# Kernel tuning notes

Measured on AMD Instinct MI355X. Metric: run time of the kernel, lower is better.

## Reference

```python
import jax, jax.numpy as jnp
import numpy as np

TEMPERATURE = 0.1
NEG_INF = -1e30

def _normalize(v):
    # torch.nn.functional.normalize: v / max(||v||, 1e-12)
    n = jnp.linalg.norm(v, axis=-1, keepdims=True)
    return v / jnp.maximum(n, 1e-12)

def _line_loss(xn, yn, mx, my):
    # xn, yn: [T, D] normalized; mx, my: [T] {0,1} combined selection masks
    T = xn.shape[0]
    sim = (xn @ yn.T) / TEMPERATURE                     # [T, T]
    nx = jnp.sum(mx)
    ny = jnp.sum(my)
    # stable argsort puts selected indices first, preserving original order
    r = jnp.argsort(1 - mx)
    c = jnp.argsort(1 - my)
    sim_sel = sim[r][:, c]                              # selected block is top-left [nx, ny]
    ids = jnp.arange(T)
    masked = jnp.where((ids < nx)[:, None], sim_sel, NEG_INF)
    lse = jax.nn.logsumexp(masked, axis=0)              # column logsumexp over selected rows
    per = lse - jnp.diagonal(sim_sel)                   # = -log(exp(diag)/sum_col exp)
    m = jnp.minimum(nx, ny)                             # torch.diag length of [nx, ny] matrix
    return jnp.sum(jnp.where(ids < m, per, 0.0)) / m

def setup_inputs() -> dict:
    key = jax.random.key(0)
    k1, k2, k3, k4 = jax.random.split(key, 4)
    B, T, D = 8, 4096, 64
    x = jax.random.normal(k1, (B, T, D), dtype=jnp.float32)
    y = jax.random.normal(k2, (B, T, D), dtype=jnp.float32)
    image_masks1 = jax.random.randint(k3, (B, T), 0, 2).astype(jnp.int32)
    image_masks2 = jax.random.randint(k4, (B, T), 0, 2).astype(jnp.int32)
    shift_masks1 = jnp.ones((B, T), dtype=jnp.int32)
    shift_masks2 = jnp.ones((B, T), dtype=jnp.int32)
    return {"x": x, "y": y, "image_masks1": image_masks1, "image_masks2": image_masks2,
            "shift_masks1": shift_masks1, "shift_masks2": shift_masks2}

def reference(x, y, image_masks1, image_masks2, shift_masks1, shift_masks2):
    xn = _normalize(x)
    yn = _normalize(y)
    mx = shift_masks1 * image_masks1   # combined row selection (shift then image)
    my = shift_masks2 * image_masks2   # combined col selection
    losses = jax.vmap(_line_loss)(xn, yn, mx, my)  # [B]
    return jnp.mean(losses)
```

## Files before the change

### kernel.cpp

```cpp
#include <hip/hip_runtime.h>
#include <hip/hip_bf16.h>
#include <math.h>

#define T_DIM 4096
#define D_DIM 64
#define SPLITS 4
#define ROWS_PER_SPLIT (T_DIM / SPLITS)
#define ITERS (ROWS_PER_SPLIT / 64)

typedef short bfrag8 __attribute__((ext_vector_type(8)));
typedef float floatx4 __attribute__((ext_vector_type(4)));

__device__ __forceinline__ float bf2f(unsigned short u) {
    return __uint_as_float(((unsigned int)u) << 16);
}

__global__ void normalize_rows(const float* __restrict__ x, const float* __restrict__ y,
                               __hip_bfloat16* __restrict__ xn, __hip_bfloat16* __restrict__ yn,
                               int rows_per_tensor) {
    int gtid = blockIdx.x * blockDim.x + threadIdx.x;
    int row  = gtid >> 6;
    int lane = gtid & 63;
    const float* src; __hip_bfloat16* dst; float scale;
    if (row < rows_per_tensor) { src = x; dst = xn; scale = 10.0f; }
    else { src = y; dst = yn; scale = 1.0f; row -= rows_per_tensor; }
    size_t off = (size_t)row * D_DIM + lane;
    float v = src[off];
    float ss = v * v;
    #pragma unroll
    for (int o = 1; o < 64; o <<= 1) ss += __shfl_xor(ss, o);
    float inv = scale / fmaxf(sqrtf(ss), 1e-12f);
    dst[off] = __float2bfloat16(v * inv);
}

__global__ void compact_mask(const int* __restrict__ im1, const int* __restrict__ sh1,
                             const int* __restrict__ im2, const int* __restrict__ sh2,
                             int* __restrict__ Ridx, int* __restrict__ Cidx,
                             float* __restrict__ mxf, int* __restrict__ cnt, int B) {
    int z = blockIdx.x;
    int which = z & 1, b = z >> 1;
    const int* im = which ? im2 : im1;
    const int* sh = which ? sh2 : sh1;
    int* idxout   = which ? Cidx : Ridx;

    __shared__ int wtot[16];
    __shared__ int woff[16];
    __shared__ int sbase;
    int tid = threadIdx.x, w = tid >> 6, lane = tid & 63;
    if (tid == 0) sbase = 0;

    for (int chunk = 0; chunk < T_DIM; chunk += 1024) {
        int t = chunk + tid;
        int mv = im[(size_t)b * T_DIM + t] * sh[(size_t)b * T_DIM + t];
        unsigned long long bal = __ballot(mv != 0);
        int pre = __popcll(bal & ((1ull << lane) - 1ull));
        if (lane == 0) wtot[w] = __popcll(bal);
        __syncthreads();
        if (tid == 0) {
            int s = sbase;
            #pragma unroll
            for (int i = 0; i < 16; i++) { woff[i] = s; s += wtot[i]; }
            sbase = s;
        }
        __syncthreads();
        if (mv) idxout[(size_t)b * T_DIM + woff[w] + pre] = t;
        if (which == 0) mxf[(size_t)b * T_DIM + t] = (mv != 0) ? 1.0f : 0.0f;
    }
    __syncthreads();
    if (tid == 0) cnt[which * B + b] = sbase;
}

__launch_bounds__(256)
__global__ void ntxent_main(const __hip_bfloat16* __restrict__ xn,
                            const __hip_bfloat16* __restrict__ yn,
                            const float* __restrict__ mxf,
                            const int* __restrict__ Cidx,
                            const int* __restrict__ cnt,
                            float* __restrict__ gsum, int B) {
    int b  = blockIdx.y;
    int nx = cnt[b];
    int ny = cnt[B + b];
    int m  = min(nx, ny);
    int j0 = blockIdx.x * 64;
    if (j0 >= m) return;
    int rbase = blockIdx.z * ROWS_PER_SPLIT;

    __shared__ __hip_bfloat16 Bs[64 * 72];
    __shared__ float sum_exp[64];
    __shared__ int   Cloc[64];

    int tid  = threadIdx.x;
    int wave = tid >> 6, lane = tid & 63, quad = lane >> 4, c16 = lane & 15;

    if (tid < 64) {
        int j = j0 + tid;
        Cloc[tid]    = (j < ny) ? Cidx[(size_t)b * T_DIM + j] : 0;
        sum_exp[tid] = 0.0f;
    }
    __syncthreads();

    #pragma unroll
    for (int i = tid; i < 64 * 8; i += 256) {
        int c = i >> 3, part = i & 7;
        bfrag8 v = *reinterpret_cast<const bfrag8*>(
            yn + ((size_t)b * T_DIM + Cloc[c]) * D_DIM + part * 8);
        *reinterpret_cast<bfrag8*>(&Bs[c * 72 + part * 8]) = v;
    }
    __syncthreads();

    bfrag8 bf[4][2];
    #pragma unroll
    for (int cg = 0; cg < 4; cg++)
        #pragma unroll
        for (int kh = 0; kh < 2; kh++)
            bf[cg][kh] = *reinterpret_cast<const bfrag8*>(
                &Bs[(cg * 16 + c16) * 72 + kh * 32 + quad * 8]);

    const __hip_bfloat16* xb = xn + (size_t)b * T_DIM * D_DIM;
    const float* mb = mxf + (size_t)b * T_DIM;

    float csum[4] = {0.f, 0.f, 0.f, 0.f};

    const __hip_bfloat16* arow = xb + (size_t)(rbase + wave * 16 + c16) * D_DIM;
    bfrag8 af0 = *reinterpret_cast<const bfrag8*>(arow + quad * 8);
    bfrag8 af1 = *reinterpret_cast<const bfrag8*>(arow + 32 + quad * 8);
    float4 mv  = *reinterpret_cast<const float4*>(mb + rbase + wave * 16 + quad * 4);

    for (int it = 0; it < ITERS; it++) {
        int it1 = (it + 1) & (ITERS - 1);
        const __hip_bfloat16* narow =
            xb + (size_t)(rbase + it1 * 64 + wave * 16 + c16) * D_DIM;
        bfrag8 naf0 = *reinterpret_cast<const bfrag8*>(narow + quad * 8);
        bfrag8 naf1 = *reinterpret_cast<const bfrag8*>(narow + 32 + quad * 8);
        float4 nmv  = *reinterpret_cast<const float4*>(
            mb + rbase + it1 * 64 + wave * 16 + quad * 4);

        float mvv[4] = {mv.x, mv.y, mv.z, mv.w};
        #pragma unroll
        for (int cg = 0; cg < 4; cg++) {
            floatx4 acc = {0.f, 0.f, 0.f, 0.f};
            acc = __builtin_amdgcn_mfma_f32_16x16x32_bf16(af0, bf[cg][0], acc, 0, 0, 0);
            acc = __builtin_amdgcn_mfma_f32_16x16x32_bf16(af1, bf[cg][1], acc, 0, 0, 0);
            #pragma unroll
            for (int r = 0; r < 4; r++)
                csum[cg] += mvv[r] * __expf(acc[r]);
        }
        af0 = naf0; af1 = naf1; mv = nmv;
    }

    #pragma unroll
    for (int cg = 0; cg < 4; cg++) {
        csum[cg] += __shfl_xor(csum[cg], 16);
        csum[cg] += __shfl_xor(csum[cg], 32);
    }
    if (lane < 16) {
        #pragma unroll
        for (int cg = 0; cg < 4; cg++)
            atomicAdd(&sum_exp[cg * 16 + c16], csum[cg]);
    }
    __syncthreads();

    if (tid < 64)
        atomicAdd(&gsum[(size_t)b * T_DIM + j0 + tid], sum_exp[tid]);
}

__global__ void per_col_loss(const __hip_bfloat16* __restrict__ xn,
                             const __hip_bfloat16* __restrict__ yn,
                             const float* __restrict__ gsum,
                             const int* __restrict__ Ridx, const int* __restrict__ Cidx,
                             const int* __restrict__ cnt,
                             float* __restrict__ partial, int B) {
    int b  = blockIdx.y;
    int nx = cnt[b];
    int ny = cnt[B + b];
    int m  = min(nx, ny);
    if (blockIdx.x * 16 >= m) return;

    int tid = threadIdx.x, wave = tid >> 6, lane = tid & 63;
    int g = tid >> 4, l = tid & 15;
    int j = blockIdx.x * 16 + g;

    float per = 0.0f;
    if (j < m) {
        int rj = Ridx[(size_t)b * T_DIM + j];
        int cj = Cidx[(size_t)b * T_DIM + j];
        const unsigned short* xa =
            (const unsigned short*)(xn + ((size_t)b * T_DIM + rj) * D_DIM) + l * 4;
        const unsigned short* yc =
            (const unsigned short*)(yn + ((size_t)b * T_DIM + cj) * D_DIM) + l * 4;
        float d = 0.0f;
        #pragma unroll
        for (int e = 0; e < 4; e++) d += bf2f(xa[e]) * bf2f(yc[e]);
        #pragma unroll
        for (int o = 1; o < 16; o <<= 1) d += __shfl_xor(d, o);
        per = (l == 0) ? (logf(gsum[(size_t)b * T_DIM + j]) - d) : 0.0f;
    }
    #pragma unroll
    for (int o = 1; o < 64; o <<= 1) per += __shfl_xor(per, o);
    __shared__ float ws[4];
    if (lane == 0) ws[wave] = per;
    __syncthreads();
    if (tid == 0) atomicAdd(&partial[b], ws[0] + ws[1] + ws[2] + ws[3]);
}

__global__ void finalize_loss(const float* __restrict__ partial, const int* __restrict__ cnt,
                              float* __restrict__ out, int B) {
    if (threadIdx.x == 0) {
        float acc = 0.0f;
        for (int b = 0; b < B; b++) {
            int mm = min(cnt[b], cnt[B + b]);
            if (mm > 0) acc += partial[b] / (float)mm;
        }
        out[0] = acc / (float)B;
    }
}

extern "C" void kernel_launch(void* const* d_in, const int* in_sizes, int n_in,
                              void* d_out, int out_size, void* d_ws, size_t ws_size,
                              hipStream_t stream) {
    const float* x  = (const float*)d_in[0];
    const float* y  = (const float*)d_in[1];
    const int* im1  = (const int*)d_in[2];
    const int* im2  = (const int*)d_in[3];
    const int* sh1  = (const int*)d_in[4];
    const int* sh2  = (const int*)d_in[5];

    int B = in_sizes[2] / T_DIM;
    size_t nElem = (size_t)B * T_DIM * D_DIM;

    __hip_bfloat16* xn = (__hip_bfloat16*)d_ws;
    __hip_bfloat16* yn = xn + nElem;
    float* mxf  = (float*)(yn + nElem);
    float* gsum = mxf + (size_t)B * T_DIM;
    float* partial = gsum + (size_t)B * T_DIM;
    int*   Ridx = (int*)(partial + B);
    int*   Cidx = Ridx + (size_t)B * T_DIM;
    int*   cnt  = Cidx + (size_t)B * T_DIM;

    hipMemsetAsync(gsum, 0, ((size_t)B * T_DIM + B) * sizeof(float), stream);

    int rows = B * T_DIM;
    int totalThreads = 2 * rows * 64;
    normalize_rows<<<totalThreads / 256, 256, 0, stream>>>(x, y, xn, yn, rows);

    compact_mask<<<2 * B, 1024, 0, stream>>>(im1, sh1, im2, sh2, Ridx, Cidx, mxf, cnt, B);

    dim3 grid(T_DIM / 64, B, SPLITS);
    ntxent_main<<<grid, 256, 0, stream>>>(xn, yn, mxf, Cidx, cnt, gsum, B);

    dim3 grid2(T_DIM / 16, B);
    per_col_loss<<<grid2, 256, 0, stream>>>(xn, yn, gsum, Ridx, Cidx, cnt, partial, B);

    finalize_loss<<<1, 64, 0, stream>>>(partial, cnt, (float*)d_out, B);
}
```

Baseline: 132.2 us.

## Fuse normalize and mask compaction into one prep kernel, use exp2 domain

Merges the normalize and mask-compaction kernels into one launch that vectorizes normalization (float4 loads, 16 lanes per row) and zeroes gsum and the output, which removes the memset. It folds log2(e) into the x scale so the main loop can use exp2f and the final loss uses log2 times ln2. It doubles the row splits in the main kernel for more parallelism at the cost of more atomics. It also drops the finalize kernel by having a grid-strided per-column loss kernel atomically add normalized partials into the output. Together these cut the launch count from five plus a memset to three.

```diff
diff --git a/kernel.cpp b/kernel.cpp
--- a/kernel.cpp
+++ b/kernel.cpp
@@ -4,9 +4,11 @@
 
 #define T_DIM 4096
 #define D_DIM 64
-#define SPLITS 4
+#define SPLITS 8
 #define ROWS_PER_SPLIT (T_DIM / SPLITS)
 #define ITERS (ROWS_PER_SPLIT / 64)
+#define SCALE_X 14.4269504088896340736f
+#define LN2 0.69314718055994530942f
 
 typedef short bfrag8 __attribute__((ext_vector_type(8)));
 typedef float floatx4 __attribute__((ext_vector_type(4)));
@@ -15,59 +17,73 @@
     return __uint_as_float(((unsigned int)u) << 16);
 }
 
-__global__ void normalize_rows(const float* __restrict__ x, const float* __restrict__ y,
-                               __hip_bfloat16* __restrict__ xn, __hip_bfloat16* __restrict__ yn,
-                               int rows_per_tensor) {
-    int gtid = blockIdx.x * blockDim.x + threadIdx.x;
-    int row  = gtid >> 6;
-    int lane = gtid & 63;
-    const float* src; __hip_bfloat16* dst; float scale;
-    if (row < rows_per_tensor) { src = x; dst = xn; scale = 10.0f; }
-    else { src = y; dst = yn; scale = 1.0f; row -= rows_per_tensor; }
-    size_t off = (size_t)row * D_DIM + lane;
-    float v = src[off];
-    float ss = v * v;
-    #pragma unroll
-    for (int o = 1; o < 64; o <<= 1) ss += __shfl_xor(ss, o);
-    float inv = scale / fmaxf(sqrtf(ss), 1e-12f);
-    dst[off] = __float2bfloat16(v * inv);
-}
-
-__global__ void compact_mask(const int* __restrict__ im1, const int* __restrict__ sh1,
-                             const int* __restrict__ im2, const int* __restrict__ sh2,
-                             int* __restrict__ Ridx, int* __restrict__ Cidx,
-                             float* __restrict__ mxf, int* __restrict__ cnt, int B) {
-    int z = blockIdx.x;
-    int which = z & 1, b = z >> 1;
-    const int* im = which ? im2 : im1;
-    const int* sh = which ? sh2 : sh1;
-    int* idxout   = which ? Cidx : Ridx;
-
-    __shared__ int wtot[16];
-    __shared__ int woff[16];
-    __shared__ int sbase;
-    int tid = threadIdx.x, w = tid >> 6, lane = tid & 63;
-    if (tid == 0) sbase = 0;
-
-    for (int chunk = 0; chunk < T_DIM; chunk += 1024) {
-        int t = chunk + tid;
-        int mv = im[(size_t)b * T_DIM + t] * sh[(size_t)b * T_DIM + t];
-        unsigned long long bal = __ballot(mv != 0);
-        int pre = __popcll(bal & ((1ull << lane) - 1ull));
-        if (lane == 0) wtot[w] = __popcll(bal);
-        __syncthreads();
-        if (tid == 0) {
-            int s = sbase;
-            #pragma unroll
-            for (int i = 0; i < 16; i++) { woff[i] = s; s += wtot[i]; }
-            sbase = s;
+__launch_bounds__(256)
+__global__ void prep(const float* __restrict__ x, const float* __restrict__ y,
+                     const int* __restrict__ im1, const int* __restrict__ sh1,
+                     const int* __restrict__ im2, const int* __restrict__ sh2,
+                     __hip_bfloat16* __restrict__ xn, __hip_bfloat16* __restrict__ yn,
+                     float* __restrict__ mxf, int* __restrict__ Ridx, int* __restrict__ Cidx,
+                     int* __restrict__ cnt, float* __restrict__ gsum, float* __restrict__ out,
+                     int rows, int normBlocks, int B) {
+    int tid = threadIdx.x;
+    if ((int)blockIdx.x < normBlocks) {
+        int row = blockIdx.x * 16 + (tid >> 4);
+        int l = tid & 15;
+        const float* src; __hip_bfloat16* dst; float scale;
+        if (row < rows) { src = x; dst = xn; scale = SCALE_X; }
+        else { src = y; dst = yn; scale = 1.0f; row -= rows; }
+        size_t off = (size_t)row * D_DIM + l * 4;
+        float4 v = *reinterpret_cast<const float4*>(src + off);
+        float ss = v.x * v.x + v.y * v.y + v.z * v.z + v.w * v.w;
+        #pragma unroll
+        for (int o = 1; o < 16; o <<= 1) ss += __shfl_xor(ss, o);
+        float inv = scale / fmaxf(sqrtf(ss), 1e-12f);
+        __hip_bfloat16 h0 = __float2bfloat16(v.x * inv);
+        __hip_bfloat16 h1 = __float2bfloat16(v.y * inv);
+        __hip_bfloat16 h2 = __float2bfloat16(v.z * inv);
+        __hip_bfloat16 h3 = __float2bfloat16(v.w * inv);
+        ushort4 o4;
+        o4.x = *reinterpret_cast<unsigned short*>(&h0);
+        o4.y = *reinterpret_cast<unsigned short*>(&h1);
+        o4.z = *reinterpret_cast<unsigned short*>(&h2);
+        o4.w = *reinterpret_cast<unsigned short*>(&h3);
+        *reinterpret_cast<ushort4*>((unsigned short*)dst + off) = o4;
+    } else {
+        int z = blockIdx.x - normBlocks;
+        int which = z & 1, b = z >> 1;
+        const int* im = which ? im2 : im1;
+        const int* sh = which ? sh2 : sh1;
+        int* idxout   = which ? Cidx : Ridx;
+
+        __shared__ int wtot[4], woff[4];
+        __shared__ int sbase;
+        int w = tid >> 6, lane = tid & 63;
+        if (tid == 0) sbase = 0;
+
+        for (int chunk = 0; chunk < T_DIM; chunk += 256) {
+            int t = chunk + tid;
+            int mv = im[(size_t)b * T_DIM + t] * sh[(size_t)b * T_DIM + t];
+            unsigned long long bal = __ballot(mv != 0);
+            int pre = __popcll(bal & ((1ull << lane) - 1ull));
+            if (lane == 0) wtot[w] = __popcll(bal);
+            __syncthreads();
+            if (tid == 0) {
+                int s = sbase;
+                #pragma unroll
+                for (int i = 0; i < 4; i++) { woff[i] = s; s += wtot[i]; }
+                sbase = s;
+            }
+            __syncthreads();
+            if (mv) idxout[(size_t)b * T_DIM + woff[w] + pre] = t;
+            if (which == 0) mxf[(size_t)b * T_DIM + t] = (mv != 0) ? 1.0f : 0.0f;
         }
         __syncthreads();
-        if (mv) idxout[(size_t)b * T_DIM + woff[w] + pre] = t;
-        if (which == 0) mxf[(size_t)b * T_DIM + t] = (mv != 0) ? 1.0f : 0.0f;
-    }
-    __syncthreads();
-    if (tid == 0) cnt[which * B + b] = sbase;
+        if (tid == 0) cnt[which * B + b] = sbase;
+        if (which == 0) {
+            for (int i = tid; i < T_DIM; i += 256) gsum[(size_t)b * T_DIM + i] = 0.0f;
+            if (z == 0 && tid == 0) out[0] = 0.0f;
+        }
+    }
 }
 
 __launch_bounds__(256)
@@ -78,9 +94,8 @@
                             const int* __restrict__ cnt,
                             float* __restrict__ gsum, int B) {
     int b  = blockIdx.y;
-    int nx = cnt[b];
     int ny = cnt[B + b];
-    int m  = min(nx, ny);
+    int m  = min(cnt[b], ny);
     int j0 = blockIdx.x * 64;
     if (j0 >= m) return;
     int rbase = blockIdx.z * ROWS_PER_SPLIT;
@@ -143,7 +158,7 @@
             acc = __builtin_amdgcn_mfma_f32_16x16x32_bf16(af1, bf[cg][1], acc, 0, 0, 0);
             #pragma unroll
             for (int r = 0; r < 4; r++)
-                csum[cg] += mvv[r] * __expf(acc[r]);
+                csum[cg] += mvv[r] * exp2f(acc[r]);
         }
         af0 = naf0; af1 = naf1; mv = nmv;
     }
@@ -164,24 +179,22 @@
         atomicAdd(&gsum[(size_t)b * T_DIM + j0 + tid], sum_exp[tid]);
 }
 
+__launch_bounds__(256)
 __global__ void per_col_loss(const __hip_bfloat16* __restrict__ xn,
                              const __hip_bfloat16* __restrict__ yn,
                              const float* __restrict__ gsum,
                              const int* __restrict__ Ridx, const int* __restrict__ Cidx,
                              const int* __restrict__ cnt,
-                             float* __restrict__ partial, int B) {
+                             float* __restrict__ out, int B) {
     int b  = blockIdx.y;
-    int nx = cnt[b];
-    int ny = cnt[B + b];
-    int m  = min(nx, ny);
-    if (blockIdx.x * 16 >= m) return;
+    int m  = min(cnt[b], cnt[B + b]);
+    if (m <= 0) return;
 
     int tid = threadIdx.x, wave = tid >> 6, lane = tid & 63;
     int g = tid >> 4, l = tid & 15;
-    int j = blockIdx.x * 16 + g;
-
-    float per = 0.0f;
-    if (j < m) {
+
+    float acc = 0.0f;
+    for (int j = blockIdx.x * 16 + g; j < m; j += 16 * gridDim.x) {
         int rj = Ridx[(size_t)b * T_DIM + j];
         int cj = Cidx[(size_t)b * T_DIM + j];
         const unsigned short* xa =
@@ -193,26 +206,15 @@
         for (int e = 0; e < 4; e++) d += bf2f(xa[e]) * bf2f(yc[e]);
         #pragma unroll
         for (int o = 1; o < 16; o <<= 1) d += __shfl_xor(d, o);
-        per = (l == 0) ? (logf(gsum[(size_t)b * T_DIM + j]) - d) : 0.0f;
-    }
-    #pragma unroll
-    for (int o = 1; o < 64; o <<= 1) per += __shfl_xor(per, o);
+        if (l == 0) acc += LN2 * (__log2f(gsum[(size_t)b * T_DIM + j]) - d);
+    }
+    #pragma unroll
+    for (int o = 1; o < 64; o <<= 1) acc += __shfl_xor(acc, o);
     __shared__ float ws[4];
-    if (lane == 0) ws[wave] = per;
-    __syncthreads();
-    if (tid == 0) atomicAdd(&partial[b], ws[0] + ws[1] + ws[2] + ws[3]);
-}
-
-__global__ void finalize_loss(const float* __restrict__ partial, const int* __restrict__ cnt,
-                              float* __restrict__ out, int B) {
-    if (threadIdx.x == 0) {
-        float acc = 0.0f;
-        for (int b = 0; b < B; b++) {
-            int mm = min(cnt[b], cnt[B + b]);
-            if (mm > 0) acc += partial[b] / (float)mm;
-        }
-        out[0] = acc / (float)B;
-    }
+    if (lane == 0) ws[wave] = acc;
+    __syncthreads();
+    if (tid == 0)
+        atomicAdd(out, (ws[0] + ws[1] + ws[2] + ws[3]) / ((float)m * (float)B));
 }
 
 extern "C" void kernel_launch(void* const* d_in, const int* in_sizes, int n_in,
@@ -226,30 +228,26 @@
     const int* sh2  = (const int*)d_in[5];
 
     int B = in_sizes[2] / T_DIM;
-    size_t nElem = (size_t)B * T_DIM * D_DIM;
+    int rows = B * T_DIM;
+    size_t nElem = (size_t)rows * D_DIM;
 
     __hip_bfloat16* xn = (__hip_bfloat16*)d_ws;
     __hip_bfloat16* yn = xn + nElem;
     float* mxf  = (float*)(yn + nElem);
-    float* gsum = mxf + (size_t)B * T_DIM;
-    float* partial = gsum + (size_t)B * T_DIM;
-    int*   Ridx = (int*)(partial + B);
-    int*   Cidx = Ridx + (size_t)B * T_DIM;
-    int*   cnt  = Cidx + (size_t)B * T_DIM;
-
-    hipMemsetAsync(gsum, 0, ((size_t)B * T_DIM + B) * sizeof(float), stream);
-
-    int rows = B * T_DIM;
-    int totalThreads = 2 * rows * 64;
-    normalize_rows<<<totalThreads / 256, 256, 0, stream>>>(x, y, xn, yn, rows);
-
-    compact_mask<<<2 * B, 1024, 0, stream>>>(im1, sh1, im2, sh2, Ridx, Cidx, mxf, cnt, B);
+    float* gsum = mxf + (size_t)rows;
+    int*   Ridx = (int*)(gsum + rows);
+    int*   Cidx = Ridx + rows;
+    int*   cnt  = Cidx + rows;
+
+    int normBlocks = 2 * rows / 16;
+    prep<<<normBlocks + 2 * B, 256, 0, stream>>>(x, y, im1, sh1, im2, sh2,
+                                                 xn, yn, mxf, Ridx, Cidx, cnt,
+                                                 gsum, (float*)d_out, rows, normBlocks, B);
 
     dim3 grid(T_DIM / 64, B, SPLITS);
     ntxent_main<<<grid, 256, 0, stream>>>(xn, yn, mxf, Cidx, cnt, gsum, B);
 
-    dim3 grid2(T_DIM / 16, B);
-    per_col_loss<<<grid2, 256, 0, stream>>>(xn, yn, gsum, Ridx, Cidx, cnt, partial, B);
-
-    finalize_loss<<<1, 64, 0, stream>>>(partial, cnt, (float*)d_out, B);
-}
+    dim3 grid2(16, B);
+    per_col_loss<<<grid2, 256, 0, stream>>>(xn, yn, gsum, Ridx, Cidx, cnt,
+                                            (float*)d_out, B);
+}
```

After: 120.6 us. -8.8%, faster.
